# Optimization experiments

Measured on AMD Instinct MI355X. Metric: run time of the kernel, lower is better.

The kernel has to match this reference:

```python
import jax, jax.numpy as jnp
import numpy as np
import math

EMBED_DIM = 256
NUM_HEADS = 8
NUM_LEVELS = 4
NUM_POINTS = 4
HEAD_DIM = EMBED_DIM // NUM_HEADS
SPATIAL_SHAPES = np.array([[100, 100], [50, 50], [25, 25], [13, 13]], dtype=np.int64)
LEN_V = int((SPATIAL_SHAPES[:, 0] * SPATIAL_SHAPES[:, 1]).sum())  # 13294
BS, LEN_Q = 8, 1024


def _grid_sample_bilinear(img, grid):
    """img: [N, C, H, W]; grid: [N, Hg, Wg, 2] in [-1,1].
    bilinear, padding_mode='zeros', align_corners=False. Returns [N, Hg, Wg, C]."""
    N, C, H, W = img.shape
    x = (grid[..., 0] + 1.0) * (W * 0.5) - 0.5
    y = (grid[..., 1] + 1.0) * (H * 0.5) - 0.5
    x0 = jnp.floor(x)
    y0 = jnp.floor(y)
    x1 = x0 + 1.0
    y1 = y0 + 1.0
    wx1 = x - x0
    wx0 = 1.0 - wx1
    wy1 = y - y0
    wy0 = 1.0 - wy1
    b = jnp.arange(N)[:, None, None]

    def gather(yi, xi):
        valid = (yi >= 0) & (yi <= H - 1) & (xi >= 0) & (xi <= W - 1)
        yc = jnp.clip(yi, 0, H - 1).astype(jnp.int32)
        xc = jnp.clip(xi, 0, W - 1).astype(jnp.int32)
        v = img[b, :, yc, xc]  # [N, Hg, Wg, C]
        return v * valid[..., None].astype(img.dtype)

    out = (gather(y0, x0) * (wy0 * wx0)[..., None]
           + gather(y0, x1) * (wy0 * wx1)[..., None]
           + gather(y1, x0) * (wy1 * wx0)[..., None]
           + gather(y1, x1) * (wy1 * wx1)[..., None])
    return out


def _offset_bias_init():
    # Faithful to _reset_parameters: per-head directional grid init for offsets bias.
    thetas = np.arange(NUM_HEADS, dtype=np.float32) * (2.0 * math.pi / NUM_HEADS)
    g = np.stack([np.cos(thetas), np.sin(thetas)], -1)
    g = g / np.abs(g).max(-1, keepdims=True)
    g = np.tile(g.reshape(NUM_HEADS, 1, 1, 2), (1, NUM_LEVELS, NUM_POINTS, 1))
    g = g * np.arange(1, NUM_POINTS + 1, dtype=np.float32).reshape(1, 1, -1, 1)
    return jnp.asarray(g.reshape(-1))


def setup_inputs() -> dict:
    key = jax.random.key(0)
    ks = jax.random.split(key, 8)
    TP = NUM_HEADS * NUM_LEVELS * NUM_POINTS  # 128

    def xavier(k, fan_in, fan_out):
        lim = math.sqrt(6.0 / (fan_in + fan_out))
        return jax.random.uniform(k, (fan_in, fan_out), jnp.float32, -lim, lim)

    return {
        "query": jax.random.normal(ks[0], (BS, LEN_Q, EMBED_DIM), jnp.float32),
        "reference_points": jax.random.uniform(ks[1], (BS, LEN_Q, NUM_LEVELS, 2), jnp.float32),
        "value": jax.random.normal(ks[2], (BS, LEN_V, EMBED_DIM), jnp.float32),
        "value_spatial_shapes": SPATIAL_SHAPES,
        # small random weights (instead of the zero-init) so the math paths are exercised
        "so_w": 0.01 * jax.random.normal(ks[3], (EMBED_DIM, TP * 2), jnp.float32),
        "so_b": _offset_bias_init(),
        "aw_w": 0.01 * jax.random.normal(ks[4], (EMBED_DIM, TP), jnp.float32),
        "aw_b": jnp.zeros((TP,), jnp.float32),
        "vp_w": xavier(ks[5], EMBED_DIM, EMBED_DIM),
        "vp_b": jnp.zeros((EMBED_DIM,), jnp.float32),
        "op_w": xavier(ks[6], EMBED_DIM, EMBED_DIM),
        "op_b": jnp.zeros((EMBED_DIM,), jnp.float32),
    }


def reference(query, reference_points, value, value_spatial_shapes,
              so_w, so_b, aw_w, aw_b, vp_w, vp_b, op_w, op_b):
    shapes = np.asarray(value_spatial_shapes)  # static python ints
    bs, len_q, D = query.shape
    H, L, P, hd = NUM_HEADS, NUM_LEVELS, NUM_POINTS, HEAD_DIM

    v = value @ vp_w + vp_b                              # [bs, len_v, D]
    v = v.reshape(bs, -1, H, hd)                         # [bs, len_v, H, hd]

    so = (query @ so_w + so_b).reshape(bs, len_q, H, L, P, 2)
    aw = (query @ aw_w + aw_b).reshape(bs, len_q, H, L * P)
    aw = jax.nn.softmax(aw, axis=-1).reshape(bs, len_q, H, L, P)

    # reference_points last dim == 2 branch: normalize offsets by (w, h) per level
    norm = jnp.asarray(shapes[:, ::-1].copy(), dtype=query.dtype).reshape(1, 1, 1, L, 1, 2)
    loc = reference_points.reshape(bs, len_q, 1, L, 1, 2) + so / norm
    grids = 2.0 * loc - 1.0                              # [bs, len_q, H, L, P, 2]
    grids = grids.transpose(0, 2, 1, 3, 4, 5).reshape(bs * H, len_q, L, P, 2)

    samples = []
    start = 0
    for lvl in range(L):
        h, w = int(shapes[lvl, 0]), int(shapes[lvl, 1])
        vl = v[:, start:start + h * w]                   # [bs, hw, H, hd]
        start += h * w
        img = vl.transpose(0, 2, 3, 1).reshape(bs * H, hd, h, w)
        s = _grid_sample_bilinear(img, grids[:, :, lvl])  # [bs*H, len_q, P, hd]
        samples.append(s)
    samp = jnp.stack(samples, axis=2)                    # [bs*H, len_q, L, P, hd]

    w_ = aw.transpose(0, 2, 1, 3, 4).reshape(bs * H, len_q, L, P)
    out = jnp.einsum('nqlpd,nqlp->nqd', samp, w_)        # [bs*H, len_q, hd]
    out = out.reshape(bs, H, len_q, hd).transpose(0, 2, 1, 3).reshape(bs, len_q, D)
    return out @ op_w + op_b
```

## Files before the change

### kernel.cpp

```cpp
#include <hip/hip_runtime.h>
#include <hip/hip_bf16.h>
#include <math.h>

#define BSZ 8
#define LQ  1024
#define LV  13294
#define NH  8
#define HD  32
#define VM  (BSZ * LV)

typedef __attribute__((ext_vector_type(8))) short bf16x8;
typedef __attribute__((ext_vector_type(4))) float f32x4;

__device__ static inline unsigned short f2bf(float f) {
    unsigned int u = __float_as_uint(f);
    unsigned int r = (u + 0x7FFFu + ((u >> 16) & 1u)) >> 16;
    return (unsigned short)r;
}
__device__ static inline float bf2f(unsigned short s) {
    return __uint_as_float(((unsigned int)s) << 16);
}
__device__ static inline unsigned int pk2bf(float a, float b) {
    __hip_bfloat162 h = __float22bfloat162_rn(make_float2(a, b));
    return *(unsigned int*)&h;
}

__global__ __launch_bounds__(256) void wconv_kernel(
    const float* __restrict__ w0, const float* __restrict__ w1,
    unsigned short* __restrict__ t0, unsigned short* __restrict__ t1)
{
    const int n = blockIdx.x & 255;
    const int k = threadIdx.x;
    if (blockIdx.x < 256) {
        const int kc = k >> 5, kk = k & 31;
        t0[((kc * 256 + n) << 5) + kk] = f2bf(w0[k * 256 + n]);
    } else {
        t1[n * 256 + k] = f2bf(w1[k * 256 + n]);
    }
}

__global__ __launch_bounds__(256, 4) void vproj_mfma_kernel(
    const float* __restrict__ A,
    const unsigned short* __restrict__ wT,
    const float* __restrict__ bias,
    unsigned short* __restrict__ v)
{
    __shared__ __align__(16) unsigned short Asb[64 * 256];

    const int tid  = threadIdx.x;
    const int w    = tid >> 6;
    const int lane = tid & 63;
    const int mrow = lane & 15;
    const int quad = lane >> 4;
    const int m0   = blockIdx.x * 64;

#pragma unroll
    for (int r = 0; r < 16; ++r) {
        const int flat = r * 256 + tid;
        const int grow = flat >> 6;
        const int gcol = flat & 63;
        int gm = m0 + grow; if (gm >= VM) gm = VM - 1;
        const float4 f = *(const float4*)(A + (size_t)gm * 256 + gcol * 4);
        uint2 pk;
        pk.x = pk2bf(f.x, f.y);
        pk.y = pk2bf(f.z, f.w);
        const int c  = gcol >> 1;
        const int cp = c ^ (grow & 31);
        *(uint2*)&Asb[grow * 256 + cp * 8 + (gcol & 1) * 4] = pk;
    }
    __syncthreads();

    f32x4 acc[4][4];
#pragma unroll
    for (int i = 0; i < 4; ++i)
#pragma unroll
        for (int j = 0; j < 4; ++j) acc[i][j] = (f32x4)0.f;

#pragma unroll
    for (int kc = 0; kc < 8; ++kc) {
        bf16x8 wfr[4], af[4];
#pragma unroll
        for (int j = 0; j < 4; ++j) {
            const int n = w * 64 + j * 16 + mrow;
            wfr[j] = *(const bf16x8*)(const void*)(wT + (((size_t)kc * 256 + n) << 5) + quad * 8);
        }
#pragma unroll
        for (int i = 0; i < 4; ++i) {
            const int mr = i * 16 + mrow;
            const int cp = (kc * 4 + quad) ^ (mr & 31);
            af[i] = *(const bf16x8*)(const void*)&Asb[mr * 256 + cp * 8];
        }
#pragma unroll
        for (int i = 0; i < 4; ++i)
#pragma unroll
            for (int j = 0; j < 4; ++j)
                acc[i][j] = __builtin_amdgcn_mfma_f32_16x16x32_bf16(
                    wfr[j], af[i], acc[i][j], 0, 0, 0);
    }

    float4 bj[4];
#pragma unroll
    for (int j = 0; j < 4; ++j)
        bj[j] = *(const float4*)(bias + w * 64 + j * 16 + quad * 4);

#pragma unroll
    for (int i = 0; i < 4; ++i) {
        const int gm = m0 + i * 16 + mrow;
        if (gm >= VM) continue;
        const unsigned int b   = (unsigned int)gm / (unsigned int)LV;
        const unsigned int pix = (unsigned int)gm - b * (unsigned int)LV;
#pragma unroll
        for (int j = 0; j < 4; ++j) {
            const int ch = w * 64 + j * 16 + quad * 4;
            const int h  = ch >> 5, cc = ch & 31;
            uint2 o;
            o.x = pk2bf(acc[i][j][0] + bj[j].x, acc[i][j][1] + bj[j].y);
            o.y = pk2bf(acc[i][j][2] + bj[j].z, acc[i][j][3] + bj[j].w);
            *(uint2*)(v + (((size_t)(b * NH + h)) * LV + pix) * HD + cc) = o;
        }
    }
}

__global__ __launch_bounds__(512, 2) void oproj_mfma_kernel(
    const unsigned short* __restrict__ Ah,
    const unsigned short* __restrict__ opT,
    const float* __restrict__ bias,
    float* __restrict__ out)
{
    const int tid  = threadIdx.x;
    const int w    = tid >> 6;
    const int lane = tid & 63;
    const int mrow = lane & 15;
    const int quad = lane >> 4;
    const int m0   = blockIdx.x * 32;

    float4 bj[2];
#pragma unroll
    for (int j = 0; j < 2; ++j)
        bj[j] = *(const float4*)(bias + w * 32 + j * 16 + quad * 4);

    f32x4 acc[2][2];
#pragma unroll
    for (int i = 0; i < 2; ++i)
#pragma unroll
        for (int j = 0; j < 2; ++j) acc[i][j] = (f32x4)0.f;

#pragma unroll
    for (int kc = 0; kc < 8; ++kc) {
        bf16x8 wf[2], af[2];
#pragma unroll
        for (int j = 0; j < 2; ++j) {
            const int n = w * 32 + j * 16 + mrow;
            wf[j] = *(const bf16x8*)(const void*)(opT + (size_t)n * 256 + kc * 32 + quad * 8);
        }
#pragma unroll
        for (int i = 0; i < 2; ++i) {
            const int gm = m0 + i * 16 + mrow;
            af[i] = *(const bf16x8*)(const void*)(Ah + (size_t)gm * 256 + kc * 32 + quad * 8);
        }
#pragma unroll
        for (int i = 0; i < 2; ++i)
#pragma unroll
            for (int j = 0; j < 2; ++j)
                acc[i][j] = __builtin_amdgcn_mfma_f32_16x16x32_bf16(
                    wf[j], af[i], acc[i][j], 0, 0, 0);
    }

#pragma unroll
    for (int i = 0; i < 2; ++i) {
        const int gm = m0 + i * 16 + mrow;
#pragma unroll
        for (int j = 0; j < 2; ++j) {
            float4 o;
            o.x = acc[i][j][0] + bj[j].x;
            o.y = acc[i][j][1] + bj[j].y;
            o.z = acc[i][j][2] + bj[j].z;
            o.w = acc[i][j][3] + bj[j].w;
            *(float4*)(out + (size_t)gm * 256 + w * 32 + j * 16 + quad * 4) = o;
        }
    }
}

__global__ __launch_bounds__(256) void qproj_kernel(
    const float* __restrict__ A,
    const float* __restrict__ so_w, const float* __restrict__ so_b,
    const float* __restrict__ aw_w, const float* __restrict__ aw_b,
    float* __restrict__ so_raw, float* __restrict__ aw_raw)
{
    __shared__ float As[16][68];
    __shared__ float Ws[16][68];

    const int tid = threadIdx.x;
    const int tx = tid & 15, ty = tid >> 4;
    const int m0 = blockIdx.y * 64;
    const int n0g = blockIdx.x * 64;

    const float* W; const float* bias; float* C; int N, n0;
    if (n0g < 256) { W = so_w; bias = so_b; C = so_raw; N = 256; n0 = n0g; }
    else           { W = aw_w; bias = aw_b; C = aw_raw; N = 128; n0 = n0g - 256; }

    const int ra = tid >> 2;
    const int ka = (tid & 3) << 2;
    const int rw = tid >> 4;
    const int cw = (tid & 15) << 2;

    float acc[4][4];
#pragma unroll
    for (int i = 0; i < 4; ++i)
#pragma unroll
        for (int j = 0; j < 4; ++j) acc[i][j] = 0.f;

    for (int k0 = 0; k0 < 256; k0 += 16) {
        const float4 av = *(const float4*)(A + (size_t)(m0 + ra) * 256 + (k0 + ka));
        As[ka + 0][ra] = av.x;
        As[ka + 1][ra] = av.y;
        As[ka + 2][ra] = av.z;
        As[ka + 3][ra] = av.w;
        *(float4*)&Ws[rw][cw] =
            *(const float4*)(W + (size_t)(k0 + rw) * N + (n0 + cw));
        __syncthreads();
#pragma unroll
        for (int k = 0; k < 16; ++k) {
            const float4 a4 = *(const float4*)&As[k][ty << 2];
            const float4 b4 = *(const float4*)&Ws[k][tx << 2];
            const float aa[4] = {a4.x, a4.y, a4.z, a4.w};
            const float bb[4] = {b4.x, b4.y, b4.z, b4.w};
#pragma unroll
            for (int i = 0; i < 4; ++i)
#pragma unroll
                for (int j = 0; j < 4; ++j)
                    acc[i][j] = fmaf(aa[i], bb[j], acc[i][j]);
        }
        __syncthreads();
    }

#pragma unroll
    for (int i = 0; i < 4; ++i) {
        const int row = m0 + (ty << 2) + i;
#pragma unroll
        for (int j = 0; j < 4; ++j) {
            const int col = n0 + (tx << 2) + j;
            C[(size_t)row * N + col] = acc[i][j] + bias[col];
        }
    }
}

__global__ __launch_bounds__(256) void sample_kernel(
    const unsigned short* __restrict__ v,
    const float* __restrict__ so_raw,
    const float* __restrict__ aw_raw,
    const float* __restrict__ refp,
    unsigned short* __restrict__ out_head)
{
    const int blk = blockIdx.x;
    const int xcd = blk & 7;
    const int j   = blk >> 3;
    const int bh  = xcd * 8 + (j >> 8);
    const int qg  = j & 255;
    const int b   = bh >> 3;
    const int h   = bh & 7;

    const int wv   = threadIdx.x >> 6;
    const int lane = threadIdx.x & 63;
    const int ch   = lane & 7;
    const int pz   = lane >> 3;

    const int q  = qg * 4 + wv;
    const int rq = b * LQ + q;

    const float l0 = aw_raw[rq * 128 + h * 16 + pz];
    const float l1 = aw_raw[rq * 128 + h * 16 + 8 + pz];
    float mx = fmaxf(l0, l1);
    mx = fmaxf(mx, __shfl_xor(mx, 8));
    mx = fmaxf(mx, __shfl_xor(mx, 16));
    mx = fmaxf(mx, __shfl_xor(mx, 32));
    const float e0 = __expf(l0 - mx), e1 = __expf(l1 - mx);
    float sm = e0 + e1;
    sm += __shfl_xor(sm, 8);
    sm += __shfl_xor(sm, 16);
    sm += __shfl_xor(sm, 32);
    const float inv_s = 1.f / sm;

    const unsigned short* vb = v + (size_t)bh * (LV * HD) + ch * 4;

    float a0 = 0.f, a1 = 0.f, a2 = 0.f, a3 = 0.f;

#pragma unroll
    for (int r = 0; r < 2; ++r) {
        const int pt = r * 8 + pz;
        const int l  = pt >> 2;
        const int p  = pt & 3;
        const float wgt = (r ? e1 : e0) * inv_s;

        const int Wl = (l == 0) ? 100 : (l == 1) ? 50 : (l == 2) ? 25 : 13;
        const int st = (l == 0) ? 0 : (l == 1) ? 10000 : (l == 2) ? 12500 : 13125;
        const float invW = (l == 0) ? 0.01f : (l == 1) ? 0.02f : (l == 2) ? 0.04f
                                            : (1.0f / 13.0f);
        const float fw = (float)Wl;

        const float2 rxy = *(const float2*)(refp + (size_t)rq * 8 + l * 2);
        const float2 sxy = *(const float2*)(so_raw + (size_t)rq * 256 + h * 32 + l * 8 + p * 2);

        const float x = (rxy.x + sxy.x * invW) * fw - 0.5f;
        const float y = (rxy.y + sxy.y * invW) * fw - 0.5f;

        const float xf = floorf(x), yf = floorf(y);
        const int x0 = (int)xf, y0 = (int)yf;
        const float wx1 = x - xf, wx0 = 1.f - wx1;
        const float wy1 = y - yf, wy0 = 1.f - wy1;

        const float vx0 = (x0 >= 0 && x0 < Wl) ? 1.f : 0.f;
        const float vx1 = (x0 + 1 >= 0 && x0 + 1 < Wl) ? 1.f : 0.f;
        const float vy0 = (y0 >= 0 && y0 < Wl) ? 1.f : 0.f;
        const float vy1 = (y0 + 1 >= 0 && y0 + 1 < Wl) ? 1.f : 0.f;

        const int xc0 = min(max(x0, 0), Wl - 1);
        const int xc1 = min(max(x0 + 1, 0), Wl - 1);
        const int yc0 = min(max(y0, 0), Wl - 1);
        const int yc1 = min(max(y0 + 1, 0), Wl - 1);

        const float w00 = wgt * wy0 * wx0 * vy0 * vx0;
        const float w01 = wgt * wy0 * wx1 * vy0 * vx1;
        const float w10 = wgt * wy1 * wx0 * vy1 * vx0;
        const float w11 = wgt * wy1 * wx1 * vy1 * vx1;

        const int row0 = (st + yc0 * Wl) * HD;
        const int row1 = (st + yc1 * Wl) * HD;

        const ushort4 u00 = *(const ushort4*)(vb + row0 + xc0 * HD);
        const ushort4 u01 = *(const ushort4*)(vb + row0 + xc1 * HD);
        const ushort4 u10 = *(const ushort4*)(vb + row1 + xc0 * HD);
        const ushort4 u11 = *(const ushort4*)(vb + row1 + xc1 * HD);

        a0 = fmaf(w00, bf2f(u00.x), a0);
        a1 = fmaf(w00, bf2f(u00.y), a1);
        a2 = fmaf(w00, bf2f(u00.z), a2);
        a3 = fmaf(w00, bf2f(u00.w), a3);
        a0 = fmaf(w01, bf2f(u01.x), a0);
        a1 = fmaf(w01, bf2f(u01.y), a1);
        a2 = fmaf(w01, bf2f(u01.z), a2);
        a3 = fmaf(w01, bf2f(u01.w), a3);
        a0 = fmaf(w10, bf2f(u10.x), a0);
        a1 = fmaf(w10, bf2f(u10.y), a1);
        a2 = fmaf(w10, bf2f(u10.z), a2);
        a3 = fmaf(w10, bf2f(u10.w), a3);
        a0 = fmaf(w11, bf2f(u11.x), a0);
        a1 = fmaf(w11, bf2f(u11.y), a1);
        a2 = fmaf(w11, bf2f(u11.z), a2);
        a3 = fmaf(w11, bf2f(u11.w), a3);
    }

    a0 += __shfl_xor(a0, 8);  a1 += __shfl_xor(a1, 8);
    a2 += __shfl_xor(a2, 8);  a3 += __shfl_xor(a3, 8);
    a0 += __shfl_xor(a0, 16); a1 += __shfl_xor(a1, 16);
    a2 += __shfl_xor(a2, 16); a3 += __shfl_xor(a3, 16);
    a0 += __shfl_xor(a0, 32); a1 += __shfl_xor(a1, 32);
    a2 += __shfl_xor(a2, 32); a3 += __shfl_xor(a3, 32);

    if (pz == 0) {
        uint2 o;
        o.x = pk2bf(a0, a1);
        o.y = pk2bf(a2, a3);
        *(uint2*)(out_head + (size_t)rq * 256 + (h << 5) + (ch << 2)) = o;
    }
}

extern "C" void kernel_launch(void* const* d_in, const int* in_sizes, int n_in,
                              void* d_out, int out_size, void* d_ws, size_t ws_size,
                              hipStream_t stream)
{
    const float* query = (const float*)d_in[0];
    const float* refp  = (const float*)d_in[1];
    const float* value = (const float*)d_in[2];
    const float* so_w  = (const float*)d_in[4];
    const float* so_b  = (const float*)d_in[5];
    const float* aw_w  = (const float*)d_in[6];
    const float* aw_b  = (const float*)d_in[7];
    const float* vp_w  = (const float*)d_in[8];
    const float* vp_b  = (const float*)d_in[9];
    const float* op_w  = (const float*)d_in[10];
    const float* op_b  = (const float*)d_in[11];
    float* out = (float*)d_out;

    float* ws = (float*)d_ws;
    size_t off = 0;
    unsigned short* v = (unsigned short*)(ws + off);
    off += (size_t)BSZ * NH * LV * HD / 2;
    unsigned short* wTv = (unsigned short*)(ws + off); off += 32768;
    unsigned short* wTo = (unsigned short*)(ws + off); off += 32768;
    float* so_raw = ws + off; off += (size_t)BSZ * LQ * 256;
    float* aw_raw = ws + off; off += (size_t)BSZ * LQ * 128;
    unsigned short* out_head = (unsigned short*)(ws + off);
    off += (size_t)BSZ * LQ * 256 / 2;

    wconv_kernel<<<512, 256, 0, stream>>>(vp_w, op_w, wTv, wTo);

    vproj_mfma_kernel<<<(VM + 63) / 64, 256, 0, stream>>>(value, wTv, vp_b, v);

    {
        dim3 grid(6, BSZ * LQ / 64);
        qproj_kernel<<<grid, 256, 0, stream>>>(query, so_w, so_b, aw_w, aw_b,
                                               so_raw, aw_raw);
    }
    sample_kernel<<<BSZ * NH * LQ / 4, 256, 0, stream>>>(
        v, so_raw, aw_raw, refp, out_head);

    oproj_mfma_kernel<<<BSZ * LQ / 32, 512, 0, stream>>>(out_head, wTo, op_b, out);
}
```

Before: 265.4 us.

## Move query projections to split-bf16 MFMA and unify GEMM kernels

Replaces the fp32 FMA query projection (sampling offsets and attention weights) with MFMA bf16 GEMMs. The query is split into hi/lo bf16 parts so the result keeps close to fp32 accuracy. A prep kernel converts all weights and the query up front, the output projection reuses a shared 16-row templated GEMM, and the value projection tile shrinks to 32 rows for higher occupancy. This adds a conversion pass and two extra launches, and the split needs twice the MFMA work.

```diff
diff --git a/kernel.cpp b/kernel.cpp
--- a/kernel.cpp
+++ b/kernel.cpp
@@ -8,6 +8,7 @@
 #define NH  8
 #define HD  32
 #define VM  (BSZ * LV)
+#define MQ  (BSZ * LQ)
 
 typedef __attribute__((ext_vector_type(8))) short bf16x8;
 typedef __attribute__((ext_vector_type(4))) float f32x4;
@@ -25,37 +26,58 @@
     return *(unsigned int*)&h;
 }
 
-__global__ __launch_bounds__(256) void wconv_kernel(
-    const float* __restrict__ w0, const float* __restrict__ w1,
-    unsigned short* __restrict__ t0, unsigned short* __restrict__ t1)
-{
-    const int n = blockIdx.x & 255;
-    const int k = threadIdx.x;
-    if (blockIdx.x < 256) {
-        const int kc = k >> 5, kk = k & 31;
-        t0[((kc * 256 + n) << 5) + kk] = f2bf(w0[k * 256 + n]);
+__global__ __launch_bounds__(256) void prep_kernel(
+    const float* __restrict__ vp_w, const float* __restrict__ op_w,
+    const float* __restrict__ so_w, const float* __restrict__ aw_w,
+    const float* __restrict__ query,
+    unsigned short* __restrict__ wTv, unsigned short* __restrict__ wTo,
+    unsigned short* __restrict__ wTso, unsigned short* __restrict__ wTaw,
+    unsigned short* __restrict__ qhi, unsigned short* __restrict__ qlo)
+{
+    const int blk = blockIdx.x;
+    const int t   = threadIdx.x;
+    if (blk < 768) {
+        const int n = blk & 255;
+        const int k = t;
+        const float* w; unsigned short* o;
+        if      (blk < 256) { w = vp_w; o = wTv; }
+        else if (blk < 512) { w = op_w; o = wTo; }
+        else                { w = so_w; o = wTso; }
+        o[(((k >> 5) * 256 + n) << 5) + (k & 31)] = f2bf(w[k * 256 + n]);
+    } else if (blk < 896) {
+        const int n = blk - 768;
+        const int k = t;
+        wTaw[(((k >> 5) * 128 + n) << 5) + (k & 31)] = f2bf(aw_w[k * 128 + n]);
     } else {
-        t1[n * 256 + k] = f2bf(w1[k * 256 + n]);
-    }
-}
-
-__global__ __launch_bounds__(256, 4) void vproj_mfma_kernel(
+        const int idx = (blk - 896) * 256 + t;
+        const float4 f = *(const float4*)(query + (size_t)idx * 4);
+        ushort4 hi, lo;
+        hi.x = f2bf(f.x); lo.x = f2bf(f.x - bf2f(hi.x));
+        hi.y = f2bf(f.y); lo.y = f2bf(f.y - bf2f(hi.y));
+        hi.z = f2bf(f.z); lo.z = f2bf(f.z - bf2f(hi.z));
+        hi.w = f2bf(f.w); lo.w = f2bf(f.w - bf2f(hi.w));
+        *(ushort4*)(qhi + (size_t)idx * 4) = hi;
+        *(ushort4*)(qlo + (size_t)idx * 4) = lo;
+    }
+}
+
+__global__ __launch_bounds__(256, 8) void vproj_mfma_kernel(
     const float* __restrict__ A,
     const unsigned short* __restrict__ wT,
     const float* __restrict__ bias,
     unsigned short* __restrict__ v)
 {
-    __shared__ __align__(16) unsigned short Asb[64 * 256];
+    __shared__ __align__(16) unsigned short Asb[32 * 256];
 
     const int tid  = threadIdx.x;
     const int w    = tid >> 6;
     const int lane = tid & 63;
     const int mrow = lane & 15;
     const int quad = lane >> 4;
-    const int m0   = blockIdx.x * 64;
-
-#pragma unroll
-    for (int r = 0; r < 16; ++r) {
+    const int m0   = blockIdx.x * 32;
+
+#pragma unroll
+    for (int r = 0; r < 8; ++r) {
         const int flat = r * 256 + tid;
         const int grow = flat >> 6;
         const int gcol = flat & 63;
@@ -70,28 +92,28 @@
     }
     __syncthreads();
 
-    f32x4 acc[4][4];
-#pragma unroll
-    for (int i = 0; i < 4; ++i)
+    f32x4 acc[2][4];
+#pragma unroll
+    for (int i = 0; i < 2; ++i)
 #pragma unroll
         for (int j = 0; j < 4; ++j) acc[i][j] = (f32x4)0.f;
 
 #pragma unroll
     for (int kc = 0; kc < 8; ++kc) {
-        bf16x8 wfr[4], af[4];
+        bf16x8 wfr[4], af[2];
 #pragma unroll
         for (int j = 0; j < 4; ++j) {
             const int n = w * 64 + j * 16 + mrow;
             wfr[j] = *(const bf16x8*)(const void*)(wT + (((size_t)kc * 256 + n) << 5) + quad * 8);
         }
 #pragma unroll
-        for (int i = 0; i < 4; ++i) {
+        for (int i = 0; i < 2; ++i) {
             const int mr = i * 16 + mrow;
             const int cp = (kc * 4 + quad) ^ (mr & 31);
             af[i] = *(const bf16x8*)(const void*)&Asb[mr * 256 + cp * 8];
         }
 #pragma unroll
-        for (int i = 0; i < 4; ++i)
+        for (int i = 0; i < 2; ++i)
 #pragma unroll
             for (int j = 0; j < 4; ++j)
                 acc[i][j] = __builtin_amdgcn_mfma_f32_16x16x32_bf16(
@@ -104,7 +126,7 @@
         bj[j] = *(const float4*)(bias + w * 64 + j * 16 + quad * 4);
 
 #pragma unroll
-    for (int i = 0; i < 4; ++i) {
+    for (int i = 0; i < 2; ++i) {
         const int gm = m0 + i * 16 + mrow;
         if (gm >= VM) continue;
         const unsigned int b   = (unsigned int)gm / (unsigned int)LV;
@@ -121,127 +143,75 @@
     }
 }
 
-__global__ __launch_bounds__(512, 2) void oproj_mfma_kernel(
-    const unsigned short* __restrict__ Ah,
-    const unsigned short* __restrict__ opT,
+template<int NJ, bool SPLIT>
+__global__ __launch_bounds__(256) void gemm16_kernel(
+    const unsigned short* __restrict__ A,
+    const unsigned short* __restrict__ A2,
+    const unsigned short* __restrict__ wT,
     const float* __restrict__ bias,
-    float* __restrict__ out)
-{
+    float* __restrict__ C)
+{
+    constexpr int N = NJ * 64;
+    __shared__ __align__(16) unsigned short Ah[16 * 256];
+    __shared__ __align__(16) unsigned short Al[SPLIT ? 16 * 256 : 8];
+
     const int tid  = threadIdx.x;
     const int w    = tid >> 6;
     const int lane = tid & 63;
     const int mrow = lane & 15;
     const int quad = lane >> 4;
-    const int m0   = blockIdx.x * 32;
-
-    float4 bj[2];
-#pragma unroll
-    for (int j = 0; j < 2; ++j)
-        bj[j] = *(const float4*)(bias + w * 32 + j * 16 + quad * 4);
-
-    f32x4 acc[2][2];
-#pragma unroll
-    for (int i = 0; i < 2; ++i)
-#pragma unroll
-        for (int j = 0; j < 2; ++j) acc[i][j] = (f32x4)0.f;
+    const int m0   = blockIdx.x * 16;
+
+#pragma unroll
+    for (int r = 0; r < 2; ++r) {
+        const int flat = r * 256 + tid;
+        const int row  = flat >> 5;
+        const int ck   = flat & 31;
+        const int cp   = ck ^ row;
+        *(uint4*)&Ah[row * 256 + cp * 8] =
+            *(const uint4*)(A + (size_t)(m0 + row) * 256 + ck * 8);
+        if (SPLIT)
+            *(uint4*)&Al[row * 256 + cp * 8] =
+                *(const uint4*)(A2 + (size_t)(m0 + row) * 256 + ck * 8);
+    }
+    __syncthreads();
+
+    f32x4 acc[NJ];
+#pragma unroll
+    for (int j = 0; j < NJ; ++j) acc[j] = (f32x4)0.f;
 
 #pragma unroll
     for (int kc = 0; kc < 8; ++kc) {
-        bf16x8 wf[2], af[2];
-#pragma unroll
-        for (int j = 0; j < 2; ++j) {
-            const int n = w * 32 + j * 16 + mrow;
-            wf[j] = *(const bf16x8*)(const void*)(opT + (size_t)n * 256 + kc * 32 + quad * 8);
-        }
-#pragma unroll
-        for (int i = 0; i < 2; ++i) {
-            const int gm = m0 + i * 16 + mrow;
-            af[i] = *(const bf16x8*)(const void*)(Ah + (size_t)gm * 256 + kc * 32 + quad * 8);
-        }
-#pragma unroll
-        for (int i = 0; i < 2; ++i)
-#pragma unroll
-            for (int j = 0; j < 2; ++j)
-                acc[i][j] = __builtin_amdgcn_mfma_f32_16x16x32_bf16(
-                    wf[j], af[i], acc[i][j], 0, 0, 0);
-    }
-
-#pragma unroll
-    for (int i = 0; i < 2; ++i) {
-        const int gm = m0 + i * 16 + mrow;
-#pragma unroll
-        for (int j = 0; j < 2; ++j) {
-            float4 o;
-            o.x = acc[i][j][0] + bj[j].x;
-            o.y = acc[i][j][1] + bj[j].y;
-            o.z = acc[i][j][2] + bj[j].z;
-            o.w = acc[i][j][3] + bj[j].w;
-            *(float4*)(out + (size_t)gm * 256 + w * 32 + j * 16 + quad * 4) = o;
-        }
-    }
-}
-
-__global__ __launch_bounds__(256) void qproj_kernel(
-    const float* __restrict__ A,
-    const float* __restrict__ so_w, const float* __restrict__ so_b,
-    const float* __restrict__ aw_w, const float* __restrict__ aw_b,
-    float* __restrict__ so_raw, float* __restrict__ aw_raw)
-{
-    __shared__ float As[16][68];
-    __shared__ float Ws[16][68];
-
-    const int tid = threadIdx.x;
-    const int tx = tid & 15, ty = tid >> 4;
-    const int m0 = blockIdx.y * 64;
-    const int n0g = blockIdx.x * 64;
-
-    const float* W; const float* bias; float* C; int N, n0;
-    if (n0g < 256) { W = so_w; bias = so_b; C = so_raw; N = 256; n0 = n0g; }
-    else           { W = aw_w; bias = aw_b; C = aw_raw; N = 128; n0 = n0g - 256; }
-
-    const int ra = tid >> 2;
-    const int ka = (tid & 3) << 2;
-    const int rw = tid >> 4;
-    const int cw = (tid & 15) << 2;
-
-    float acc[4][4];
-#pragma unroll
-    for (int i = 0; i < 4; ++i)
-#pragma unroll
-        for (int j = 0; j < 4; ++j) acc[i][j] = 0.f;
-
-    for (int k0 = 0; k0 < 256; k0 += 16) {
-        const float4 av = *(const float4*)(A + (size_t)(m0 + ra) * 256 + (k0 + ka));
-        As[ka + 0][ra] = av.x;
-        As[ka + 1][ra] = av.y;
-        As[ka + 2][ra] = av.z;
-        As[ka + 3][ra] = av.w;
-        *(float4*)&Ws[rw][cw] =
-            *(const float4*)(W + (size_t)(k0 + rw) * N + (n0 + cw));
-        __syncthreads();
-#pragma unroll
-        for (int k = 0; k < 16; ++k) {
-            const float4 a4 = *(const float4*)&As[k][ty << 2];
-            const float4 b4 = *(const float4*)&Ws[k][tx << 2];
-            const float aa[4] = {a4.x, a4.y, a4.z, a4.w};
-            const float bb[4] = {b4.x, b4.y, b4.z, b4.w};
-#pragma unroll
-            for (int i = 0; i < 4; ++i)
-#pragma unroll
-                for (int j = 0; j < 4; ++j)
-                    acc[i][j] = fmaf(aa[i], bb[j], acc[i][j]);
-        }
-        __syncthreads();
-    }
-
-#pragma unroll
-    for (int i = 0; i < 4; ++i) {
-        const int row = m0 + (ty << 2) + i;
-#pragma unroll
-        for (int j = 0; j < 4; ++j) {
-            const int col = n0 + (tx << 2) + j;
-            C[(size_t)row * N + col] = acc[i][j] + bias[col];
-        }
+        bf16x8 wf[NJ];
+#pragma unroll
+        for (int j = 0; j < NJ; ++j) {
+            const int n = w * (NJ * 16) + j * 16 + mrow;
+            wf[j] = *(const bf16x8*)(const void*)(wT + (((size_t)kc * N + n) << 5) + quad * 8);
+        }
+        const int cp = (kc * 4 + quad) ^ mrow;
+        const bf16x8 af = *(const bf16x8*)(const void*)&Ah[mrow * 256 + cp * 8];
+#pragma unroll
+        for (int j = 0; j < NJ; ++j)
+            acc[j] = __builtin_amdgcn_mfma_f32_16x16x32_bf16(wf[j], af, acc[j], 0, 0, 0);
+        if (SPLIT) {
+            const bf16x8 af2 = *(const bf16x8*)(const void*)&Al[mrow * 256 + cp * 8];
+#pragma unroll
+            for (int j = 0; j < NJ; ++j)
+                acc[j] = __builtin_amdgcn_mfma_f32_16x16x32_bf16(wf[j], af2, acc[j], 0, 0, 0);
+        }
+    }
+
+    const int gm = m0 + mrow;
+#pragma unroll
+    for (int j = 0; j < NJ; ++j) {
+        const int col = w * (NJ * 16) + j * 16 + quad * 4;
+        const float4 bb = *(const float4*)(bias + col);
+        float4 o;
+        o.x = acc[j][0] + bb.x;
+        o.y = acc[j][1] + bb.y;
+        o.z = acc[j][2] + bb.z;
+        o.w = acc[j][3] + bb.w;
+        *(float4*)(C + (size_t)gm * N + col) = o;
     }
 }
 
@@ -386,24 +356,27 @@
     size_t off = 0;
     unsigned short* v = (unsigned short*)(ws + off);
     off += (size_t)BSZ * NH * LV * HD / 2;
-    unsigned short* wTv = (unsigned short*)(ws + off); off += 32768;
-    unsigned short* wTo = (unsigned short*)(ws + off); off += 32768;
-    float* so_raw = ws + off; off += (size_t)BSZ * LQ * 256;
-    float* aw_raw = ws + off; off += (size_t)BSZ * LQ * 128;
+    unsigned short* wTv  = (unsigned short*)(ws + off); off += 32768;
+    unsigned short* wTo  = (unsigned short*)(ws + off); off += 32768;
+    unsigned short* wTso = (unsigned short*)(ws + off); off += 32768;
+    unsigned short* wTaw = (unsigned short*)(ws + off); off += 16384;
+    unsigned short* qhi  = (unsigned short*)(ws + off); off += (size_t)MQ * 128;
+    unsigned short* qlo  = (unsigned short*)(ws + off); off += (size_t)MQ * 128;
+    float* so_raw = ws + off; off += (size_t)MQ * 256;
+    float* aw_raw = ws + off; off += (size_t)MQ * 128;
     unsigned short* out_head = (unsigned short*)(ws + off);
-    off += (size_t)BSZ * LQ * 256 / 2;
-
-    wconv_kernel<<<512, 256, 0, stream>>>(vp_w, op_w, wTv, wTo);
-
-    vproj_mfma_kernel<<<(VM + 63) / 64, 256, 0, stream>>>(value, wTv, vp_b, v);
-
-    {
-        dim3 grid(6, BSZ * LQ / 64);
-        qproj_kernel<<<grid, 256, 0, stream>>>(query, so_w, so_b, aw_w, aw_b,
-                                               so_raw, aw_raw);
-    }
+    off += (size_t)MQ * 128;
+
+    prep_kernel<<<2944, 256, 0, stream>>>(vp_w, op_w, so_w, aw_w, query,
+                                          wTv, wTo, wTso, wTaw, qhi, qlo);
+
+    vproj_mfma_kernel<<<(VM + 31) / 32, 256, 0, stream>>>(value, wTv, vp_b, v);
+
+    gemm16_kernel<4, true><<<MQ / 16, 256, 0, stream>>>(qhi, qlo, wTso, so_b, so_raw);
+    gemm16_kernel<2, true><<<MQ / 16, 256, 0, stream>>>(qhi, qlo, wTaw, aw_b, aw_raw);
+
     sample_kernel<<<BSZ * NH * LQ / 4, 256, 0, stream>>>(
         v, so_raw, aw_raw, refp, out_head);
 
-    oproj_mfma_kernel<<<BSZ * LQ / 32, 512, 0, stream>>>(out_head, wTo, op_b, out);
-}
+    gemm16_kernel<4, false><<<MQ / 16, 256, 0, stream>>>(out_head, nullptr, wTo, op_b, out);
+}
```

After: 291.2 us. 9.7% more time.
